# Kernel optimization log

Measured on AMD Instinct MI355X. Metric: run time of the kernel, lower is better.

The kernel has to match this reference:

```python
import jax, jax.numpy as jnp
import numpy as np

N = 50000
E = 800000
DIM = 128


def setup_inputs() -> dict:
    key = jax.random.key(0)
    ks = jax.random.split(key, 12)
    s = 1.0 / np.sqrt(DIM)
    s2 = 1.0 / np.sqrt(2 * DIM)
    return {
        "h": jax.random.normal(ks[0], (N, DIM), dtype=jnp.float32),
        "edge_index": jax.random.randint(ks[1], (2, E), 0, N, dtype=jnp.int64),
        # msg_mlp: Linear(dim,dim) -> ReLU -> Linear(dim,dim) -> ReLU
        "W1": jax.random.uniform(ks[2], (DIM, DIM), jnp.float32, -s, s),
        "b1": jax.random.uniform(ks[3], (DIM,), jnp.float32, -s, s),
        "W2": jax.random.uniform(ks[4], (DIM, DIM), jnp.float32, -s, s),
        "b2": jax.random.uniform(ks[5], (DIM,), jnp.float32, -s, s),
        # update_mlp: Linear(2*dim,dim) -> ReLU -> Linear(dim,dim)
        "U1": jax.random.uniform(ks[6], (2 * DIM, DIM), jnp.float32, -s2, s2),
        "c1": jax.random.uniform(ks[7], (DIM,), jnp.float32, -s2, s2),
        "U2": jax.random.uniform(ks[8], (DIM, DIM), jnp.float32, -s, s),
        "c2": jax.random.uniform(ks[9], (DIM,), jnp.float32, -s, s),
    }


def reference(h, edge_index, W1, b1, W2, b2, U1, c1, U2, c2):
    row, col = edge_index[0], edge_index[1]
    # gather source features and run message MLP on edges: [E, dim]
    x = h[col]
    m = jax.nn.relu(x @ W1 + b1)
    m = jax.nn.relu(m @ W2 + b2)
    # scatter-add messages to destination nodes: [N, dim]
    agg = jax.ops.segment_sum(m, row, num_segments=h.shape[0])
    # degree normalization (bincount of row, clamped at 1)
    deg = jax.ops.segment_sum(jnp.ones((m.shape[0],), m.dtype), row, num_segments=h.shape[0])
    deg = jnp.maximum(deg, 1.0)[:, None]
    agg = agg / deg
    # update MLP on [h, agg]
    z = jnp.concatenate([h, agg], axis=1)
    z = jax.nn.relu(z @ U1 + c1)
    return z @ U2 + c2
```

## Files before the change

### kernel.cpp

```cpp
#include <hip/hip_runtime.h>
#include <cstddef>

#define NN 50000
#define EE 800000
#define DIM 128
#define CAP 128
#define CSTRIDE 16

#define PREP_BLKS 320
#define ZERO_BLKS 782
#define EDGE_BLKS 3125
#define MLP2_BLKS 3125
#define GUP_BLKS  3125

typedef __attribute__((ext_vector_type(8))) short bf16x8;
typedef __attribute__((ext_vector_type(4))) float f32x4;

__device__ __forceinline__ unsigned short f2bf(float x) {
    unsigned u = __float_as_uint(x);
    unsigned r = (u + 0x7FFFu + ((u >> 16) & 1u)) >> 16;
    return (unsigned short)r;
}

__device__ __forceinline__ float bf2f(unsigned short b) {
    return __uint_as_float((unsigned)b << 16);
}

__device__ __forceinline__ int load_idx(const void* ei, bool i64, long long i) {
    return i64 ? (int)((const long long*)ei)[i] : ((const int*)ei)[i];
}

__device__ __forceinline__ bool detect_i64_inline(const void* ei) {
    int l = threadIdx.x & 63;
    int v = ((const int*)ei)[2 * l + 1];
    return __ballot(v != 0) == 0ULL;
}

__global__ __launch_bounds__(256) void prep_zero_kernel(
    const float* __restrict__ W1, const float* __restrict__ W2,
    const float* __restrict__ U1, const float* __restrict__ U2,
    unsigned short* __restrict__ W1t, unsigned short* __restrict__ W2t,
    unsigned short* __restrict__ U1h, unsigned short* __restrict__ U1l,
    unsigned short* __restrict__ U2h, unsigned short* __restrict__ U2l,
    int* __restrict__ cnt16)
{
    int bid = blockIdx.x;
    if (bid < PREP_BLKS) {
        int idx = bid * 256 + threadIdx.x;
        if (idx < 32768) {
            int m   = idx >> 14;
            int rem = idx & 16383;
            int n = rem >> 7, k = rem & 127;
            const float* W = m ? W2 : W1;
            unsigned short* Wt = m ? W2t : W1t;
            Wt[n * DIM + k] = f2bf(W[k * DIM + n]);
        } else if (idx < 65536) {
            int r = idx - 32768;
            int k = r >> 7, n = r & 127;
            float w = U1[r];
            unsigned short hx = f2bf(w);
            U1h[n * 256 + k] = hx;
            U1l[n * 256 + k] = f2bf(w - bf2f(hx));
        } else {
            int r = idx - 65536;
            int k = r >> 7, n = r & 127;
            float w = U2[r];
            unsigned short hx = f2bf(w);
            U2h[n * 128 + k] = hx;
            U2l[n * 128 + k] = f2bf(w - bf2f(hx));
        }
    } else {
        int base = (bid - PREP_BLKS) * 1024 + threadIdx.x * 4;
        if (base + 4 <= CSTRIDE * NN) {
            *(int4*)(cnt16 + base) = (int4){0, 0, 0, 0};
        } else {
            #pragma unroll
            for (int k = 0; k < 4; ++k)
                if (base + k < CSTRIDE * NN) cnt16[base + k] = 0;
        }
    }
}

__global__ __launch_bounds__(256, 8) void bucket_mlp_kernel(
    const void* __restrict__ ei, const float* __restrict__ h,
    const unsigned short* __restrict__ W1t, const float* __restrict__ b1,
    const unsigned short* __restrict__ W2t, const float* __restrict__ b2,
    int* __restrict__ cnt16, int* __restrict__ bucket,
    unsigned short* __restrict__ Mh)
{
    __shared__ unsigned short xs[16][136];

    if (blockIdx.x < EDGE_BLKS) {
        bool i64 = detect_i64_inline(ei);
        int e = blockIdx.x * 256 + threadIdx.x;
        if (e < EE) {
            int r = load_idx(ei, i64, e);
            int c = load_idx(ei, i64, (long long)EE + e);
            int slot = atomicAdd(&cnt16[(size_t)r * CSTRIDE], 1);
            if (slot < CAP)
                __builtin_nontemporal_store(c, &bucket[(size_t)r * CAP + slot]);
        }
        return;
    }

    const int tid  = threadIdx.x;
    const int lane = tid & 63;
    const int wid  = tid >> 6;
    const int g    = lane >> 4;
    const int c    = lane & 15;
    const int half = lane >> 5;
    const int hl   = lane & 31;
    const int nbase = (blockIdx.x - EDGE_BLKS) * 16;

    #pragma unroll
    for (int pass = 0; pass < 2; ++pass) {
        int r = 4 * wid + 2 * pass + half;
        int n = nbase + r;
        float4 v = *(const float4*)(h + (size_t)n * DIM + hl * 4);
        unsigned short h0 = f2bf(v.x), h1 = f2bf(v.y), h2 = f2bf(v.z), h3 = f2bf(v.w);
        *(uint2*)&xs[r][hl * 4] =
            (uint2){(unsigned)h0 | ((unsigned)h1 << 16), (unsigned)h2 | ((unsigned)h3 << 16)};
    }
    __syncthreads();

    bf16x8 a[4];
    #pragma unroll
    for (int s = 0; s < 4; ++s)
        a[s] = *(const bf16x8*)&xs[c][s * 32 + g * 8];
    __syncthreads();

    f32x4 acc[2];
    #pragma unroll
    for (int tt = 0; tt < 2; ++tt) {
        int t = 2 * wid + tt;
        float bv = b1[t * 16 + c];
        acc[tt] = (f32x4){bv, bv, bv, bv};
    }
    #pragma unroll
    for (int tt = 0; tt < 2; ++tt) {
        int t = 2 * wid + tt;
        #pragma unroll
        for (int s = 0; s < 4; ++s) {
            bf16x8 bf = *(const bf16x8*)&W1t[(t * 16 + c) * DIM + s * 32 + g * 8];
            acc[tt] = __builtin_amdgcn_mfma_f32_16x16x32_bf16(a[s], bf, acc[tt], 0, 0, 0);
        }
    }
    #pragma unroll
    for (int tt = 0; tt < 2; ++tt) {
        int t = 2 * wid + tt;
        #pragma unroll
        for (int j = 0; j < 4; ++j)
            xs[g * 4 + j][t * 16 + c] = f2bf(fmaxf(acc[tt][j], 0.f));
    }
    __syncthreads();

    #pragma unroll
    for (int s = 0; s < 4; ++s)
        a[s] = *(const bf16x8*)&xs[c][s * 32 + g * 8];
    __syncthreads();

    #pragma unroll
    for (int tt = 0; tt < 2; ++tt) {
        int t = 2 * wid + tt;
        float bv = b2[t * 16 + c];
        acc[tt] = (f32x4){bv, bv, bv, bv};
    }
    #pragma unroll
    for (int tt = 0; tt < 2; ++tt) {
        int t = 2 * wid + tt;
        #pragma unroll
        for (int s = 0; s < 4; ++s) {
            bf16x8 bf = *(const bf16x8*)&W2t[(t * 16 + c) * DIM + s * 32 + g * 8];
            acc[tt] = __builtin_amdgcn_mfma_f32_16x16x32_bf16(a[s], bf, acc[tt], 0, 0, 0);
        }
    }
    #pragma unroll
    for (int tt = 0; tt < 2; ++tt) {
        int t = 2 * wid + tt;
        #pragma unroll
        for (int j = 0; j < 4; ++j)
            xs[g * 4 + j][t * 16 + c] = f2bf(fmaxf(acc[tt][j], 0.f));
    }
    __syncthreads();

    #pragma unroll
    for (int e = 0; e < 4; ++e) {
        int r = wid * 4 + e;
        int n = nbase + r;
        *(unsigned*)(Mh + (size_t)n * DIM + lane * 2) = *(const unsigned*)&xs[r][lane * 2];
    }
}

__global__ __launch_bounds__(256, 8) void gup4_kernel(
    const float* __restrict__ h,
    const unsigned short* __restrict__ Mh, const int* __restrict__ bucket,
    const int* __restrict__ cnt16,
    const unsigned short* __restrict__ U1h, const unsigned short* __restrict__ U1l,
    const unsigned short* __restrict__ U2h, const unsigned short* __restrict__ U2l,
    const float* __restrict__ c1, const float* __restrict__ c2,
    float* __restrict__ out)
{
    __shared__ unsigned short xa[2][16][136];
    __shared__ unsigned short xh[2][16][136];
    const int tid  = threadIdx.x;
    const int lane = tid & 63;
    const int wid  = tid >> 6;
    const int g    = lane >> 4;
    const int c    = lane & 15;
    const int half = lane >> 5;
    const int hl   = lane & 31;
    const int hb   = half << 5;
    const int nbase = blockIdx.x * 16;

    #pragma unroll 1
    for (int pass = 0; pass < 2; ++pass) {
        int r  = 4 * wid + 2 * pass + half;
        int n  = nbase + r;
        int d  = cnt16[(size_t)n * CSTRIDE];
        int dg = d < CAP ? d : CAP;
        const int* brow = bucket + (size_t)n * CAP;
        float s0 = 0.f, s1 = 0.f, s2 = 0.f, s3 = 0.f;
        #pragma unroll 1
        for (int base = 0; base < dg; base += 32) {
            int m = dg - base; if (m > 32) m = 32;
            int idx = (hl < m) ? brow[base + hl] : 0;
            int j = 0;
            for (; j + 8 <= m; j += 8) {
                uint2 u[8];
                #pragma unroll
                for (int k = 0; k < 8; ++k) {
                    int si = __shfl(idx, hb + j + k);
                    u[k] = *(const uint2*)(Mh + (size_t)si * DIM + hl * 4);
                }
                #pragma unroll
                for (int k = 0; k < 8; ++k) {
                    s0 += __uint_as_float(u[k].x << 16);
                    s1 += __uint_as_float(u[k].x & 0xFFFF0000u);
                    s2 += __uint_as_float(u[k].y << 16);
                    s3 += __uint_as_float(u[k].y & 0xFFFF0000u);
                }
            }
            for (; j < m; ++j) {
                int si = __shfl(idx, hb + j);
                uint2 u0 = *(const uint2*)(Mh + (size_t)si * DIM + hl * 4);
                s0 += __uint_as_float(u0.x << 16);
                s1 += __uint_as_float(u0.x & 0xFFFF0000u);
                s2 += __uint_as_float(u0.y << 16);
                s3 += __uint_as_float(u0.y & 0xFFFF0000u);
            }
        }
        float inv = 1.0f / fmaxf((float)d, 1.0f);
        s0 *= inv; s1 *= inv; s2 *= inv; s3 *= inv;
        unsigned short h0 = f2bf(s0), h1 = f2bf(s1), h2 = f2bf(s2), h3 = f2bf(s3);
        unsigned short l0 = f2bf(s0 - bf2f(h0)), l1 = f2bf(s1 - bf2f(h1));
        unsigned short l2 = f2bf(s2 - bf2f(h2)), l3 = f2bf(s3 - bf2f(h3));
        *(uint2*)&xa[0][r][hl * 4] =
            (uint2){(unsigned)h0 | ((unsigned)h1 << 16), (unsigned)h2 | ((unsigned)h3 << 16)};
        *(uint2*)&xa[1][r][hl * 4] =
            (uint2){(unsigned)l0 | ((unsigned)l1 << 16), (unsigned)l2 | ((unsigned)l3 << 16)};

        float4 v = *(const float4*)(h + (size_t)n * DIM + hl * 4);
        unsigned short p0 = f2bf(v.x), p1 = f2bf(v.y), p2 = f2bf(v.z), p3 = f2bf(v.w);
        unsigned short q0 = f2bf(v.x - bf2f(p0)), q1 = f2bf(v.y - bf2f(p1));
        unsigned short q2 = f2bf(v.z - bf2f(p2)), q3 = f2bf(v.w - bf2f(p3));
        *(uint2*)&xh[0][r][hl * 4] =
            (uint2){(unsigned)p0 | ((unsigned)p1 << 16), (unsigned)p2 | ((unsigned)p3 << 16)};
        *(uint2*)&xh[1][r][hl * 4] =
            (uint2){(unsigned)q0 | ((unsigned)q1 << 16), (unsigned)q2 | ((unsigned)q3 << 16)};
    }
    __syncthreads();

    f32x4 acc[2];
    #pragma unroll
    for (int tt = 0; tt < 2; ++tt) {
        int t = 2 * wid + tt;
        float bv = c1[t * 16 + c];
        acc[tt] = (f32x4){bv, bv, bv, bv};
    }
    {
        bf16x8 ah[4], al[4];
        #pragma unroll
        for (int s = 0; s < 4; ++s) {
            ah[s] = *(const bf16x8*)&xa[0][c][s * 32 + g * 8];
            al[s] = *(const bf16x8*)&xa[1][c][s * 32 + g * 8];
        }
        #pragma unroll
        for (int tt = 0; tt < 2; ++tt) {
            int t = 2 * wid + tt;
            #pragma unroll
            for (int s = 0; s < 4; ++s) {
                int kof = 128 + s * 32 + g * 8;
                bf16x8 bh = *(const bf16x8*)&U1h[(t * 16 + c) * 256 + kof];
                bf16x8 bl = *(const bf16x8*)&U1l[(t * 16 + c) * 256 + kof];
                acc[tt] = __builtin_amdgcn_mfma_f32_16x16x32_bf16(ah[s], bh, acc[tt], 0, 0, 0);
                acc[tt] = __builtin_amdgcn_mfma_f32_16x16x32_bf16(al[s], bh, acc[tt], 0, 0, 0);
                acc[tt] = __builtin_amdgcn_mfma_f32_16x16x32_bf16(ah[s], bl, acc[tt], 0, 0, 0);
            }
        }
        #pragma unroll
        for (int s = 0; s < 4; ++s) {
            ah[s] = *(const bf16x8*)&xh[0][c][s * 32 + g * 8];
            al[s] = *(const bf16x8*)&xh[1][c][s * 32 + g * 8];
        }
        #pragma unroll
        for (int tt = 0; tt < 2; ++tt) {
            int t = 2 * wid + tt;
            #pragma unroll
            for (int s = 0; s < 4; ++s) {
                int kof = s * 32 + g * 8;
                bf16x8 bh = *(const bf16x8*)&U1h[(t * 16 + c) * 256 + kof];
                bf16x8 bl = *(const bf16x8*)&U1l[(t * 16 + c) * 256 + kof];
                acc[tt] = __builtin_amdgcn_mfma_f32_16x16x32_bf16(ah[s], bh, acc[tt], 0, 0, 0);
                acc[tt] = __builtin_amdgcn_mfma_f32_16x16x32_bf16(al[s], bh, acc[tt], 0, 0, 0);
                acc[tt] = __builtin_amdgcn_mfma_f32_16x16x32_bf16(ah[s], bl, acc[tt], 0, 0, 0);
            }
        }
    }
    __syncthreads();

    #pragma unroll
    for (int tt = 0; tt < 2; ++tt) {
        int t = 2 * wid + tt;
        #pragma unroll
        for (int j = 0; j < 4; ++j) {
            float yv = fmaxf(acc[tt][j], 0.f);
            unsigned short hx = f2bf(yv);
            xh[0][g * 4 + j][t * 16 + c] = hx;
            xh[1][g * 4 + j][t * 16 + c] = f2bf(yv - bf2f(hx));
        }
    }
    __syncthreads();

    bf16x8 yh[4], yl[4];
    #pragma unroll
    for (int s = 0; s < 4; ++s) {
        yh[s] = *(const bf16x8*)&xh[0][c][s * 32 + g * 8];
        yl[s] = *(const bf16x8*)&xh[1][c][s * 32 + g * 8];
    }
    f32x4 acc2[2];
    #pragma unroll
    for (int tt = 0; tt < 2; ++tt) {
        int t = 2 * wid + tt;
        float bv = c2[t * 16 + c];
        acc2[tt] = (f32x4){bv, bv, bv, bv};
    }
    #pragma unroll
    for (int tt = 0; tt < 2; ++tt) {
        int t = 2 * wid + tt;
        #pragma unroll
        for (int s = 0; s < 4; ++s) {
            int kof = s * 32 + g * 8;
            bf16x8 bh = *(const bf16x8*)&U2h[(t * 16 + c) * 128 + kof];
            bf16x8 bl = *(const bf16x8*)&U2l[(t * 16 + c) * 128 + kof];
            acc2[tt] = __builtin_amdgcn_mfma_f32_16x16x32_bf16(yh[s], bh, acc2[tt], 0, 0, 0);
            acc2[tt] = __builtin_amdgcn_mfma_f32_16x16x32_bf16(yl[s], bh, acc2[tt], 0, 0, 0);
            acc2[tt] = __builtin_amdgcn_mfma_f32_16x16x32_bf16(yh[s], bl, acc2[tt], 0, 0, 0);
        }
    }

    #pragma unroll
    for (int tt = 0; tt < 2; ++tt) {
        int t = 2 * wid + tt;
        #pragma unroll
        for (int j = 0; j < 4; ++j) {
            int n = nbase + g * 4 + j;
            out[(size_t)n * DIM + t * 16 + c] = acc2[tt][j];
        }
    }
}

__global__ void detect_i64_kernel(const int* __restrict__ ei, int* __restrict__ flag) {
    int l = threadIdx.x;
    int v = ei[2 * l + 1];
    unsigned long long b = __ballot(v != 0);
    if (l == 0) flag[0] = (b == 0ULL) ? 1 : 0;
}

__global__ __launch_bounds__(256) void prep_w_kernel(
    const float* __restrict__ W1, const float* __restrict__ W2,
    unsigned short* __restrict__ W1t, unsigned short* __restrict__ W2t)
{
    int idx = blockIdx.x * 256 + threadIdx.x;
    int m   = idx >> 14;
    int rem = idx & 16383;
    int n = rem >> 7, k = rem & 127;
    const float* W = m ? W2 : W1;
    unsigned short* Wt = m ? W2t : W1t;
    Wt[n * DIM + k] = f2bf(W[k * DIM + n]);
}

__global__ __launch_bounds__(256) void deg_i_kernel(const void* __restrict__ ei,
                                                    const int* __restrict__ flag,
                                                    int* __restrict__ deg) {
    bool i64 = flag[0] != 0;
    int e = blockIdx.x * 256 + threadIdx.x;
    if (e < EE) {
        int r = load_idx(ei, i64, e);
        atomicAdd(&deg[r], 1);
    }
}

__global__ __launch_bounds__(256) void msg_kernel(
    const float* __restrict__ h, const void* __restrict__ ei, const int* __restrict__ flag,
    const unsigned short* __restrict__ W1t, const float* __restrict__ b1,
    const unsigned short* __restrict__ W2t, const float* __restrict__ b2,
    float* __restrict__ agg)
{
    __shared__ unsigned short xs[4][16][136];
    const int tid  = threadIdx.x;
    const int lane = tid & 63;
    const int wid  = tid >> 6;
    const int g    = lane >> 4;
    const int c    = lane & 15;
    const bool i64 = flag[0] != 0;
    const int ebase = blockIdx.x * 64 + wid * 16;

    #pragma unroll
    for (int e = 0; e < 16; ++e) {
        int src = load_idx(ei, i64, (long long)EE + (ebase + e));
        float2 v = *(const float2*)(h + (size_t)src * DIM + lane * 2);
        unsigned p = (unsigned)f2bf(v.x) | ((unsigned)f2bf(v.y) << 16);
        *(unsigned*)&xs[wid][e][lane * 2] = p;
    }
    __syncthreads();

    bf16x8 a[4];
    #pragma unroll
    for (int s = 0; s < 4; ++s)
        a[s] = *(const bf16x8*)&xs[wid][c][s * 32 + g * 8];

    f32x4 acc[8];
    #pragma unroll
    for (int t = 0; t < 8; ++t) {
        float bv = b1[t * 16 + c];
        acc[t] = (f32x4){bv, bv, bv, bv};
    }
    #pragma unroll
    for (int t = 0; t < 8; ++t) {
        #pragma unroll
        for (int s = 0; s < 4; ++s) {
            bf16x8 bf = *(const bf16x8*)&W1t[(t * 16 + c) * DIM + s * 32 + g * 8];
            acc[t] = __builtin_amdgcn_mfma_f32_16x16x32_bf16(a[s], bf, acc[t], 0, 0, 0);
        }
    }
    __syncthreads();
    #pragma unroll
    for (int t = 0; t < 8; ++t)
        #pragma unroll
        for (int j = 0; j < 4; ++j)
            xs[wid][g * 4 + j][t * 16 + c] = f2bf(fmaxf(acc[t][j], 0.f));
    __syncthreads();

    #pragma unroll
    for (int s = 0; s < 4; ++s)
        a[s] = *(const bf16x8*)&xs[wid][c][s * 32 + g * 8];

    #pragma unroll
    for (int t = 0; t < 8; ++t) {
        float bv = b2[t * 16 + c];
        acc[t] = (f32x4){bv, bv, bv, bv};
    }
    #pragma unroll
    for (int t = 0; t < 8; ++t) {
        #pragma unroll
        for (int s = 0; s < 4; ++s) {
            bf16x8 bf = *(const bf16x8*)&W2t[(t * 16 + c) * DIM + s * 32 + g * 8];
            acc[t] = __builtin_amdgcn_mfma_f32_16x16x32_bf16(a[s], bf, acc[t], 0, 0, 0);
        }
    }

    #pragma unroll
    for (int j = 0; j < 4; ++j) {
        int r = load_idx(ei, i64, ebase + g * 4 + j);
        #pragma unroll
        for (int t = 0; t < 8; ++t)
            atomicAdd(&agg[(size_t)r * DIM + t * 16 + c], fmaxf(acc[t][j], 0.f));
    }
}

__global__ __launch_bounds__(256) void upd_kernel(
    const float* __restrict__ h, const float* __restrict__ aggout,
    const int* __restrict__ deg,
    const float* __restrict__ U1, const float* __restrict__ c1,
    const float* __restrict__ U2, const float* __restrict__ c2,
    float* __restrict__ out)
{
    __shared__ float zs[4][8][2 * DIM];
    const int tid  = threadIdx.x;
    const int lane = tid & 63;
    const int wid  = tid >> 6;
    const int nbase = blockIdx.x * 32 + wid * 8;

    #pragma unroll
    for (int i = 0; i < 8; ++i) {
        int n = nbase + i;
        if (n < NN) {
            float2 hv = *(const float2*)(h + (size_t)n * DIM + lane * 2);
            *(float2*)&zs[wid][i][lane * 2] = hv;
            float d = fmaxf((float)deg[n], 1.0f);
            float inv = 1.0f / d;
            float2 av = *(const float2*)(aggout + (size_t)n * DIM + lane * 2);
            av.x *= inv; av.y *= inv;
            *(float2*)&zs[wid][i][DIM + lane * 2] = av;
        }
    }
    __syncthreads();

    float acc0[8], acc1[8];
    {
        float cc0 = c1[lane], cc1 = c1[lane + 64];
        #pragma unroll
        for (int i = 0; i < 8; ++i) { acc0[i] = cc0; acc1[i] = cc1; }
    }
    for (int k = 0; k < 2 * DIM; k += 4) {
        float wa[4], wb[4];
        #pragma unroll
        for (int kk = 0; kk < 4; ++kk) {
            wa[kk] = U1[(k + kk) * DIM + lane];
            wb[kk] = U1[(k + kk) * DIM + lane + 64];
        }
        #pragma unroll
        for (int i = 0; i < 8; ++i) {
            float4 zv = *(const float4*)&zs[wid][i][k];
            acc0[i] = fmaf(zv.x, wa[0], acc0[i]);
            acc1[i] = fmaf(zv.x, wb[0], acc1[i]);
            acc0[i] = fmaf(zv.y, wa[1], acc0[i]);
            acc1[i] = fmaf(zv.y, wb[1], acc1[i]);
            acc0[i] = fmaf(zv.z, wa[2], acc0[i]);
            acc1[i] = fmaf(zv.z, wb[2], acc1[i]);
            acc0[i] = fmaf(zv.w, wa[3], acc0[i]);
            acc1[i] = fmaf(zv.w, wb[3], acc1[i]);
        }
    }
    __syncthreads();
    #pragma unroll
    for (int i = 0; i < 8; ++i) {
        zs[wid][i][lane]      = fmaxf(acc0[i], 0.f);
        zs[wid][i][lane + 64] = fmaxf(acc1[i], 0.f);
    }
    __syncthreads();

    {
        float cc0 = c2[lane], cc1 = c2[lane + 64];
        #pragma unroll
        for (int i = 0; i < 8; ++i) { acc0[i] = cc0; acc1[i] = cc1; }
    }
    for (int k = 0; k < DIM; k += 4) {
        float wa[4], wb[4];
        #pragma unroll
        for (int kk = 0; kk < 4; ++kk) {
            wa[kk] = U2[(k + kk) * DIM + lane];
            wb[kk] = U2[(k + kk) * DIM + lane + 64];
        }
        #pragma unroll
        for (int i = 0; i < 8; ++i) {
            float4 zv = *(const float4*)&zs[wid][i][k];
            acc0[i] = fmaf(zv.x, wa[0], acc0[i]);
            acc1[i] = fmaf(zv.x, wb[0], acc1[i]);
            acc0[i] = fmaf(zv.y, wa[1], acc0[i]);
            acc1[i] = fmaf(zv.y, wb[1], acc1[i]);
            acc0[i] = fmaf(zv.z, wa[2], acc0[i]);
            acc1[i] = fmaf(zv.z, wb[2], acc1[i]);
            acc0[i] = fmaf(zv.w, wa[3], acc0[i]);
            acc1[i] = fmaf(zv.w, wb[3], acc1[i]);
        }
    }

    #pragma unroll
    for (int i = 0; i < 8; ++i) {
        int n = nbase + i;
        if (n < NN) {
            out[(size_t)n * DIM + lane]      = acc0[i];
            out[(size_t)n * DIM + lane + 64] = acc1[i];
        }
    }
}

extern "C" void kernel_launch(void* const* d_in, const int* in_sizes, int n_in,
                              void* d_out, int out_size, void* d_ws, size_t ws_size,
                              hipStream_t stream) {
    const float* h  = (const float*)d_in[0];
    const void*  ei = d_in[1];
    const float* W1 = (const float*)d_in[2];
    const float* b1 = (const float*)d_in[3];
    const float* W2 = (const float*)d_in[4];
    const float* b2 = (const float*)d_in[5];
    const float* U1 = (const float*)d_in[6];
    const float* c1 = (const float*)d_in[7];
    const float* U2 = (const float*)d_in[8];
    const float* c2 = (const float*)d_in[9];
    float* out = (float*)d_out;

    const size_t BIG_BYTES = 41862144;
    const bool big = ws_size >= BIG_BYTES;

    char* wsb = (char*)d_ws;
    unsigned short *Mh, *W1t, *W2t, *U1h, *U1l, *U2h, *U2l;
    int *bucket, *cnt16, *flag;
    if (big) {
        Mh     = (unsigned short*)wsb;
        bucket = (int*)(wsb + 12800000);
        cnt16  = (int*)(wsb + 38400000);
        flag   = nullptr;
        W1t    = (unsigned short*)(wsb + 41600000);
        W2t    = (unsigned short*)(wsb + 41632768);
        U1h    = (unsigned short*)(wsb + 41665536);
        U1l    = (unsigned short*)(wsb + 41731072);
        U2h    = (unsigned short*)(wsb + 41796608);
        U2l    = (unsigned short*)(wsb + 41829376);
    } else {
        Mh     = nullptr; bucket = nullptr;
        U1h = U1l = U2h = U2l = nullptr;
        cnt16  = (int*)wsb;
        flag   = (int*)(wsb + 200000);
        W1t    = (unsigned short*)(wsb + 200064);
        W2t    = (unsigned short*)(wsb + 200064 + 32768);
    }

    if (big) {
        prep_zero_kernel<<<PREP_BLKS + ZERO_BLKS, 256, 0, stream>>>(
            W1, W2, U1, U2, W1t, W2t, U1h, U1l, U2h, U2l, cnt16);
        bucket_mlp_kernel<<<EDGE_BLKS + MLP2_BLKS, 256, 0, stream>>>(
            ei, h, W1t, b1, W2t, b2, cnt16, bucket, Mh);
        gup4_kernel<<<GUP_BLKS, 256, 0, stream>>>(h, Mh, bucket, cnt16,
                                                  U1h, U1l, U2h, U2l, c1, c2, out);
    } else {
        detect_i64_kernel<<<1, 64, 0, stream>>>((const int*)ei, flag);
        prep_w_kernel<<<128, 256, 0, stream>>>(W1, W2, W1t, W2t);
        hipMemsetAsync(cnt16, 0, (size_t)NN * sizeof(int), stream);
        deg_i_kernel<<<(EE + 255) / 256, 256, 0, stream>>>(ei, flag, cnt16);
        hipMemsetAsync(d_out, 0, (size_t)NN * DIM * sizeof(float), stream);
        msg_kernel<<<EE / 64, 256, 0, stream>>>(h, ei, flag, W1t, b1, W2t, b2, out);
        upd_kernel<<<(NN + 31) / 32, 256, 0, stream>>>(h, out, cnt16, U1, c1, U2, c2, out);
    }
}
```

Baseline: 180.8 us.

## Bucket incoming edges by source-node chunk to improve gather locality

Edges are now bucketed per destination node into 7 sub-buckets keyed by the source index range (8192 nodes each), using separate counters within the existing padded counter stride. The gather kernel walks the chunks in order, so concurrent waves tend to read message rows from the same region of Mh, aiming for better L2/cache locality. It also lowers the occupancy hint for the gather kernel and uses a masked 8-wide loop in place of the scalar tail. The trade-off is a larger bucket area, a per-chunk cap of 24 that could drop edges under skewed degree, and extra loop overhead per chunk.

```diff
diff --git a/kernel.cpp b/kernel.cpp
--- a/kernel.cpp
+++ b/kernel.cpp
@@ -4,7 +4,9 @@
 #define NN 50000
 #define EE 800000
 #define DIM 128
-#define CAP 128
+#define NCH 7
+#define CHSH 13
+#define CAPG 24
 #define CSTRIDE 16
 
 #define PREP_BLKS 320
@@ -96,9 +98,11 @@
         if (e < EE) {
             int r = load_idx(ei, i64, e);
             int c = load_idx(ei, i64, (long long)EE + e);
-            int slot = atomicAdd(&cnt16[(size_t)r * CSTRIDE], 1);
-            if (slot < CAP)
-                __builtin_nontemporal_store(c, &bucket[(size_t)r * CAP + slot]);
+            int ch = c >> CHSH;
+            int slot = atomicAdd(&cnt16[(size_t)r * CSTRIDE + ch], 1);
+            if (slot < CAPG)
+                __builtin_nontemporal_store(
+                    c, &bucket[((size_t)r * NCH + ch) * CAPG + slot]);
         }
         return;
     }
@@ -191,7 +195,7 @@
     }
 }
 
-__global__ __launch_bounds__(256, 8) void gup4_kernel(
+__global__ __launch_bounds__(256, 6) void gup4_kernel(
     const float* __restrict__ h,
     const unsigned short* __restrict__ Mh, const int* __restrict__ bucket,
     const int* __restrict__ cnt16,
@@ -216,16 +220,21 @@
     for (int pass = 0; pass < 2; ++pass) {
         int r  = 4 * wid + 2 * pass + half;
         int n  = nbase + r;
-        int d  = cnt16[(size_t)n * CSTRIDE];
-        int dg = d < CAP ? d : CAP;
-        const int* brow = bucket + (size_t)n * CAP;
+        int cv = (hl < NCH) ? cnt16[(size_t)n * CSTRIDE + hl] : 0;
+        int d = 0;
+        #pragma unroll
+        for (int gg = 0; gg < NCH; ++gg) d += __shfl(cv, hb + gg);
+
         float s0 = 0.f, s1 = 0.f, s2 = 0.f, s3 = 0.f;
         #pragma unroll 1
-        for (int base = 0; base < dg; base += 32) {
-            int m = dg - base; if (m > 32) m = 32;
-            int idx = (hl < m) ? brow[base + hl] : 0;
-            int j = 0;
-            for (; j + 8 <= m; j += 8) {
+        for (int ch = 0; ch < NCH; ++ch) {
+            int dgr = __shfl(cv, hb + ch);
+            int dg  = dgr < CAPG ? dgr : CAPG;
+            const int* brow = bucket + ((size_t)n * NCH + ch) * CAPG;
+            int chbase = ch << CHSH;
+            int idx = (hl < dg) ? brow[hl] : chbase;
+            #pragma unroll 1
+            for (int j = 0; j < dg; j += 8) {
                 uint2 u[8];
                 #pragma unroll
                 for (int k = 0; k < 8; ++k) {
@@ -234,19 +243,13 @@
                 }
                 #pragma unroll
                 for (int k = 0; k < 8; ++k) {
-                    s0 += __uint_as_float(u[k].x << 16);
-                    s1 += __uint_as_float(u[k].x & 0xFFFF0000u);
-                    s2 += __uint_as_float(u[k].y << 16);
-                    s3 += __uint_as_float(u[k].y & 0xFFFF0000u);
+                    if (j + k < dg) {
+                        s0 += __uint_as_float(u[k].x << 16);
+                        s1 += __uint_as_float(u[k].x & 0xFFFF0000u);
+                        s2 += __uint_as_float(u[k].y << 16);
+                        s3 += __uint_as_float(u[k].y & 0xFFFF0000u);
+                    }
                 }
-            }
-            for (; j < m; ++j) {
-                int si = __shfl(idx, hb + j);
-                uint2 u0 = *(const uint2*)(Mh + (size_t)si * DIM + hl * 4);
-                s0 += __uint_as_float(u0.x << 16);
-                s1 += __uint_as_float(u0.x & 0xFFFF0000u);
-                s2 += __uint_as_float(u0.y << 16);
-                s3 += __uint_as_float(u0.y & 0xFFFF0000u);
             }
         }
         float inv = 1.0f / fmaxf((float)d, 1.0f);
@@ -591,7 +594,7 @@
     const float* c2 = (const float*)d_in[9];
     float* out = (float*)d_out;
 
-    const size_t BIG_BYTES = 41862144;
+    const size_t BIG_BYTES = 49862144;
     const bool big = ws_size >= BIG_BYTES;
 
     char* wsb = (char*)d_ws;
@@ -600,14 +603,14 @@
     if (big) {
         Mh     = (unsigned short*)wsb;
         bucket = (int*)(wsb + 12800000);
-        cnt16  = (int*)(wsb + 38400000);
+        cnt16  = (int*)(wsb + 46400000);
         flag   = nullptr;
-        W1t    = (unsigned short*)(wsb + 41600000);
-        W2t    = (unsigned short*)(wsb + 41632768);
-        U1h    = (unsigned short*)(wsb + 41665536);
-        U1l    = (unsigned short*)(wsb + 41731072);
-        U2h    = (unsigned short*)(wsb + 41796608);
-        U2l    = (unsigned short*)(wsb + 41829376);
+        W1t    = (unsigned short*)(wsb + 49600000);
+        W2t    = (unsigned short*)(wsb + 49632768);
+        U1h    = (unsigned short*)(wsb + 49665536);
+        U1l    = (unsigned short*)(wsb + 49731072);
+        U2h    = (unsigned short*)(wsb + 49796608);
+        U2l    = (unsigned short*)(wsb + 49829376);
     } else {
         Mh     = nullptr; bucket = nullptr;
         U1h = U1l = U2h = U2l = nullptr;
```

New measurement: 203.7 us. +12.6%, slower.
